# Optimization experiments

Hardware: AMD Instinct MI355X
Metric: run time of the kernel (lower is better)

Reference implementation:

```python
import jax, jax.numpy as jnp
import numpy as np

ANG = 7
N = ANG * ANG          # 49 views
CENTER = N // 2        # index 24 = central view
EDGE_C = 150.0
ALPHA = 0.1
CROP = 8
GAUSS = jnp.array([[0.0751, 0.1238, 0.0751],
                   [0.1238, 0.2042, 0.1238],
                   [0.0751, 0.1238, 0.0751]], dtype=jnp.float32)


def _edge_aware_smoothness(D, I):
    # D: [b,h,w] disparity; I: [b,3,h,w] center view
    gx = I[:, :, :, 1:] - I[:, :, :, :-1]
    gy = I[:, :, 1:, :] - I[:, :, :-1, :]
    wx = jnp.exp(-EDGE_C * jnp.mean(jnp.abs(gx), axis=1, keepdims=True))
    wy = jnp.exp(-EDGE_C * jnp.mean(jnp.abs(gy), axis=1, keepdims=True))
    Du = D[:, None]
    dgx = Du[:, :, :, 1:] - Du[:, :, :, :-1]
    dgy = Du[:, :, 1:, :] - Du[:, :, :-1, :]
    lx = jnp.mean((wx * jnp.abs(dgx))[:, :, CROP:-CROP, CROP:-CROP])
    ly = jnp.mean((wy * jnp.abs(dgy))[:, :, CROP:-CROP, CROP:-CROP])
    return (lx + ly) / 2.0


def _warp_all(pred, x):
    # Backward-warp each of the 49 views toward the center view using the
    # per-pixel disparity scaled by the view's angular offset (bilinear,
    # border-clamped) -- standard light-field warping (warp_all in the repo).
    # pred: [b,h,w]; x: [b,3,N,h,w] -> warped [b,3,N,h,w]
    b, c, n, h, w = x.shape
    off = jnp.arange(ANG, dtype=pred.dtype) - (ANG // 2)
    du = jnp.repeat(off, ANG)   # row (u) offset per view, [N]
    dv = jnp.tile(off, ANG)     # col (v) offset per view, [N]
    gy = jnp.arange(h, dtype=pred.dtype)[:, None]
    gx = jnp.arange(w, dtype=pred.dtype)[None, :]
    p = pred[:, None, :, :]                                # [b,1,h,w]
    cy = jnp.clip(gy[None, None] + p * du[None, :, None, None], 0.0, h - 1)
    cx = jnp.clip(gx[None, None] + p * dv[None, :, None, None], 0.0, w - 1)
    y0f = jnp.floor(cy); x0f = jnp.floor(cx)
    ty = (cy - y0f)[..., None]; tx = (cx - x0f)[..., None]
    y0 = y0f.astype(jnp.int32); x0 = x0f.astype(jnp.int32)
    y1 = jnp.minimum(y0 + 1, h - 1); x1 = jnp.minimum(x0 + 1, w - 1)
    img = jnp.transpose(x, (0, 2, 3, 4, 1)).reshape(b, n, h * w, c)

    def gather(yi, xi):
        idx = (yi * w + xi).reshape(b, n, h * w, 1)
        return jnp.take_along_axis(img, idx, axis=2).reshape(b, n, h, w, c)

    out = (gather(y0, x0) * (1 - ty) * (1 - tx)
           + gather(y0, x1) * (1 - ty) * tx
           + gather(y1, x0) * ty * (1 - tx)
           + gather(y1, x1) * ty * tx)
    return jnp.transpose(out, (0, 4, 1, 2, 3))


def _gauss_smooth_angular(cl):
    # cl [b,1,N,h,w]: 3x3 gaussian conv over the 7x7 angular grid, replicate pad
    b, _, _, h, w = cl.shape
    g = cl.reshape(b, 1, ANG, ANG, h, w)
    g = jnp.pad(g, ((0, 0), (0, 0), (1, 1), (1, 1), (0, 0), (0, 0)), mode='edge')
    out = sum(GAUSS[i, j] * g[:, :, i:i + ANG, j:j + ANG]
              for i in range(3) for j in range(3))
    return out.reshape(b, 1, N, h, w)


def _forward(pred, x, y, epoch):
    b, u, v, h, w, c = x.shape
    # 'b u v h w c -> b c (u v) h w'
    xr = jnp.transpose(x, (0, 5, 1, 2, 3, 4)).reshape(b, c, N, h, w)
    center = xr[:, :, CENTER]                               # [b,3,h,w]
    grad_loss = _edge_aware_smoothness(pred, center)
    warped = _warp_all(pred, xr)                            # [b,3,N,h,w]
    color_loss = jnp.mean(jnp.abs(warped - warped[:, :, CENTER:CENTER + 1]),
                          axis=1, keepdims=True)            # [b,1,N,h,w]
    if epoch > 0:
        gauss = jax.lax.stop_gradient(_gauss_smooth_angular(color_loss))
        idx = jnp.argsort(-gauss, axis=2)                   # descending
        sorted_cl = jnp.take_along_axis(color_loss, idx, axis=2)
    else:
        sorted_cl = -jnp.sort(-color_loss, axis=2)
    yb = y[:, None, None, :, :]
    ar = jnp.arange(N, dtype=y.dtype)[None, None, :, None, None]
    mask = (ar > yb).astype(color_loss.dtype) / (N - yb) * N
    if epoch > 0:
        mask = jax.lax.stop_gradient(mask)                  # torch no_grad branch
    cl = jnp.mean((sorted_cl * mask)[..., CROP:-CROP, CROP:-CROP])
    return cl + grad_loss * ALPHA


def setup_inputs():
    key = jax.random.key(0)
    k1, k2, k3 = jax.random.split(key, 3)
    b, h, w = 4, 256, 256
    pred = jax.random.normal(k1, (b, h, w), dtype=jnp.float32)
    x = jax.random.uniform(k2, (b, ANG, ANG, h, w, 3), dtype=jnp.float32)
    y = jax.random.uniform(k3, (b, h, w), dtype=jnp.float32) * 24.0  # keep ~half views
    return {"pred": pred, "x": x, "y": y, "epoch": 5}


def reference(pred, x, y, epoch):
    return _forward(pred, x, y, epoch)
```

## Files before the change

### kernel.cpp

```cpp
#include <hip/hip_runtime.h>
#include <math.h>

#define NV    49
#define Himg  256
#define Wimg  256
#define RW    240
#define RWH   (RW*RW)
#define NPIX  (4*RWH)
#define ROWF  (Wimg*3)
#define IMGF  (Himg*Wimg*3)
#define NBLK  (NPIX/64)


#define CL7(a) ((a)<0?0:((a)>6?6:(a)))

#define DO_VIEW(UC, VC) { \
    const float* s0p = xv + ((UC)*7 + (VC)) * IMGF + ro0 + co[VC]; \
    const float* s1p = xv + ((UC)*7 + (VC)) * IMGF + ro1 + co[VC]; \
    float s0[6], s1[6]; \
    __builtin_memcpy(s0, s0p, 24); \
    __builtin_memcpy(s1, s1p, 24); \
    float tx = txv[VC]; \
    float h0 = s0[0] + tx*(s0[3]-s0[0]); \
    float h1 = s0[1] + tx*(s0[4]-s0[1]); \
    float h2 = s0[2] + tx*(s0[5]-s0[2]); \
    float k0 = s1[0] + tx*(s1[3]-s1[0]); \
    float k1 = s1[1] + tx*(s1[4]-s1[1]); \
    float k2 = s1[2] + tx*(s1[5]-s1[2]); \
    float o0 = h0 + ty*(k0-h0); \
    float o1 = h1 + ty*(k1-h1); \
    float o2 = h2 + ty*(k2-h2); \
    mycl[(UC)*7+(VC)] = (fabsf(o0-c0)+fabsf(o1-c1)+fabsf(o2-c2)) * (1.0f/3.0f); \
}

#define DO_U(UC) { \
    float cy = fminf(fmaxf((float)yy + p * (float)((UC)-3), 0.0f), 255.0f); \
    float y0f = floorf(cy); \
    float ty = cy - y0f; \
    int iy0 = (int)y0f; \
    int iy1 = min(iy0+1, 255); \
    int ro0 = iy0*ROWF, ro1 = iy1*ROWF; \
    DO_VIEW(UC,0) DO_VIEW(UC,1) DO_VIEW(UC,2) DO_VIEW(UC,3) \
    DO_VIEW(UC,4) DO_VIEW(UC,5) DO_VIEW(UC,6) \
}

#define GV(UC,VC) myg[(UC)*7+(VC)] = \
    0.0751f*mycl[CL7((UC)-1)*7+CL7((VC)-1)] + 0.1238f*mycl[CL7((UC)-1)*7+(VC)] + 0.0751f*mycl[CL7((UC)-1)*7+CL7((VC)+1)] + \
    0.1238f*mycl[(UC)*7+CL7((VC)-1)]        + 0.2042f*mycl[(UC)*7+(VC)]        + 0.1238f*mycl[(UC)*7+CL7((VC)+1)] + \
    0.0751f*mycl[CL7((UC)+1)*7+CL7((VC)-1)] + 0.1238f*mycl[CL7((UC)+1)*7+(VC)] + 0.0751f*mycl[CL7((UC)+1)*7+CL7((VC)+1)];

#define GU(UC) GV(UC,0) GV(UC,1) GV(UC,2) GV(UC,3) GV(UC,4) GV(UC,5) GV(UC,6)

__global__ __launch_bounds__(256) void color_kernel(
    const float* __restrict__ pred, const float* __restrict__ x,
    const float* __restrict__ y, const int* __restrict__ epoch_p,
    double* __restrict__ acc)
{
    __shared__ float s_cl[64 * NV];
    __shared__ float s_g [64 * NV];
    __shared__ float sred[4];

    const int tid = threadIdx.x;
    const int pix = tid & 63;
    const int sub = tid >> 6;

    int lb  = (blockIdx.x & 7) * (NBLK/8) + (blockIdx.x >> 3);
    int pid = lb * 64 + pix;
    int b   = pid / RWH;
    int rem = pid - b * RWH;
    int ry  = rem / RW;
    int yy  = 8 + ry;
    int xx  = 8 + (rem - ry * RW);

    int pidx = (b * Himg + yy) * Wimg + xx;
    float p = pred[pidx];

    const float* xv    = x + (size_t)b * (49 * IMGF);
    const float* cbase = xv + (24 * IMGF) + (yy * Wimg + xx) * 3;
    float c0 = cbase[0], c1 = cbase[1], c2 = cbase[2];

    float* mycl = s_cl + pix * NV;
    float* myg  = s_g  + pix * NV;

    int co[7]; float txv[7];
    #pragma unroll
    for (int vv = 0; vv < 7; vv++) {
        float cx = fminf(fmaxf((float)xx + p * (float)(vv-3), 0.0f), 255.0f);
        float x0f = floorf(cx);
        float tx = cx - x0f;
        int ix0 = (int)x0f;
        if (ix0 >= 255) { ix0 = 254; tx = 1.0f; }
        co[vv] = ix0 * 3; txv[vv] = tx;
    }

    if (sub == 0)      { DO_U(0) DO_U(4) }
    else if (sub == 1) { DO_U(1) DO_U(5) }
    else if (sub == 2) { DO_U(2) DO_U(6) }
    else {
        DO_U(3)
        float lx = 0.0f, ly = 0.0f;
        if (xx <= 246) {
            float q6[6]; __builtin_memcpy(q6, cbase, 24);
            float wx = __expf(-50.0f * (fabsf(q6[3]-c0) + fabsf(q6[4]-c1) + fabsf(q6[5]-c2)));
            lx = wx * fabsf(pred[pidx + 1] - p);
        }
        if (yy <= 246) {
            float r0 = cbase[ROWF], r1 = cbase[ROWF+1], r2 = cbase[ROWF+2];
            float wy = __expf(-50.0f * (fabsf(r0-c0) + fabsf(r1-c1) + fabsf(r2-c2)));
            ly = wy * fabsf(pred[pidx + Wimg] - p);
        }
        #pragma unroll
        for (int off = 32; off > 0; off >>= 1) {
            lx += __shfl_down(lx, off);
            ly += __shfl_down(ly, off);
        }
        if ((tid & 63) == 0) {
            atomicAdd(acc + 1, (double)lx);
            atomicAdd(acc + 2, (double)ly);
        }
    }
    __syncthreads();

    const int epoch = *epoch_p;

    if (epoch > 0) {
        if (sub == 0)      { GU(0) GU(4) }
        else if (sub == 1) { GU(1) GU(5) }
        else if (sub == 2) { GU(2) GU(6) }
        else               { GU(3) }
    }
    __syncthreads();

    const float* key = (epoch > 0) ? myg : mycl;
    float yval = y[pidx];

    unsigned long long kn[13];
    int cnt[13];
    #pragma unroll
    for (int i = 0; i < 13; i++) {
        int n = sub + 4*i;
        if (n < NV) {
            unsigned int bb = __float_as_uint(key[n]);
            kn[i] = (((unsigned long long)bb) << 8) | (unsigned long long)(255 - n);
        } else kn[i] = ~0ULL;
        cnt[i] = 0;
    }
    for (int m = 0; m < NV; m++) {
        unsigned int bm = __float_as_uint(key[m]);
        unsigned long long km = (((unsigned long long)bm) << 8) | (unsigned long long)(255 - m);
        #pragma unroll
        for (int i = 0; i < 13; i++)
            cnt[i] += (km > kn[i]) ? 1 : 0;
    }
    float tail = 0.0f;
    #pragma unroll
    for (int i = 0; i < 13; i++) {
        int n = sub + 4*i;
        if (n < NV)
            tail += ((float)cnt[i] > yval) ? mycl[n] : 0.0f;
    }
    float contrib = tail * (49.0f / (49.0f - yval));

    #pragma unroll
    for (int off = 32; off > 0; off >>= 1)
        contrib += __shfl_down(contrib, off);
    if ((tid & 63) == 0) sred[sub] = contrib;
    __syncthreads();
    if (tid == 0)
        atomicAdd(acc + 0, (double)(sred[0] + sred[1] + sred[2] + sred[3]));
}

__global__ void finalize_kernel(const double* __restrict__ acc,
                                float* __restrict__ out)
{
    double cl = acc[0] / 11289600.0;
    double gl = (acc[1] + acc[2]) / (2.0 * 229440.0);
    out[0] = (float)(cl + 0.1 * gl);
}

extern "C" void kernel_launch(void* const* d_in, const int* in_sizes, int n_in,
                              void* d_out, int out_size, void* d_ws, size_t ws_size,
                              hipStream_t stream)
{
    const float* pred  = (const float*)d_in[0];
    const float* x     = (const float*)d_in[1];
    const float* y     = (const float*)d_in[2];
    const int*   epoch = (const int*)d_in[3];
    double* acc = (double*)d_ws;

    hipMemsetAsync(acc, 0, 3 * sizeof(double), stream);
    color_kernel<<<NBLK, 256, 0, stream>>>(pred, x, y, epoch, acc);
    finalize_kernel<<<1, 1, 0, stream>>>(acc, (float*)d_out);
}
```

Measured before the change: 325.7 us.

## Use seven wavefronts per block, one per angular row, balancing work

The block grows from 4 to 7 wavefronts, so each wavefront handles exactly one angular row of 7 views for warping, Gaussian smoothing and rank counting. Before, one wavefront did one row and the other three did two rows each, which left the work unbalanced. Each wavefront's color losses stay in registers for the tail sum, and the wavefront index is made uniform with readfirstlane so the per-row loops are not compiled as divergent branches. The larger block raises threads per block and may change register pressure and occupancy.

```diff
diff --git a/kernel.cpp b/kernel.cpp
--- a/kernel.cpp
+++ b/kernel.cpp
@@ -12,57 +12,18 @@
 #define NBLK  (NPIX/64)
 
 
-#define CL7(a) ((a)<0?0:((a)>6?6:(a)))
-
-#define DO_VIEW(UC, VC) { \
-    const float* s0p = xv + ((UC)*7 + (VC)) * IMGF + ro0 + co[VC]; \
-    const float* s1p = xv + ((UC)*7 + (VC)) * IMGF + ro1 + co[VC]; \
-    float s0[6], s1[6]; \
-    __builtin_memcpy(s0, s0p, 24); \
-    __builtin_memcpy(s1, s1p, 24); \
-    float tx = txv[VC]; \
-    float h0 = s0[0] + tx*(s0[3]-s0[0]); \
-    float h1 = s0[1] + tx*(s0[4]-s0[1]); \
-    float h2 = s0[2] + tx*(s0[5]-s0[2]); \
-    float k0 = s1[0] + tx*(s1[3]-s1[0]); \
-    float k1 = s1[1] + tx*(s1[4]-s1[1]); \
-    float k2 = s1[2] + tx*(s1[5]-s1[2]); \
-    float o0 = h0 + ty*(k0-h0); \
-    float o1 = h1 + ty*(k1-h1); \
-    float o2 = h2 + ty*(k2-h2); \
-    mycl[(UC)*7+(VC)] = (fabsf(o0-c0)+fabsf(o1-c1)+fabsf(o2-c2)) * (1.0f/3.0f); \
-}
-
-#define DO_U(UC) { \
-    float cy = fminf(fmaxf((float)yy + p * (float)((UC)-3), 0.0f), 255.0f); \
-    float y0f = floorf(cy); \
-    float ty = cy - y0f; \
-    int iy0 = (int)y0f; \
-    int iy1 = min(iy0+1, 255); \
-    int ro0 = iy0*ROWF, ro1 = iy1*ROWF; \
-    DO_VIEW(UC,0) DO_VIEW(UC,1) DO_VIEW(UC,2) DO_VIEW(UC,3) \
-    DO_VIEW(UC,4) DO_VIEW(UC,5) DO_VIEW(UC,6) \
-}
-
-#define GV(UC,VC) myg[(UC)*7+(VC)] = \
-    0.0751f*mycl[CL7((UC)-1)*7+CL7((VC)-1)] + 0.1238f*mycl[CL7((UC)-1)*7+(VC)] + 0.0751f*mycl[CL7((UC)-1)*7+CL7((VC)+1)] + \
-    0.1238f*mycl[(UC)*7+CL7((VC)-1)]        + 0.2042f*mycl[(UC)*7+(VC)]        + 0.1238f*mycl[(UC)*7+CL7((VC)+1)] + \
-    0.0751f*mycl[CL7((UC)+1)*7+CL7((VC)-1)] + 0.1238f*mycl[CL7((UC)+1)*7+(VC)] + 0.0751f*mycl[CL7((UC)+1)*7+CL7((VC)+1)];
-
-#define GU(UC) GV(UC,0) GV(UC,1) GV(UC,2) GV(UC,3) GV(UC,4) GV(UC,5) GV(UC,6)
-
-__global__ __launch_bounds__(256) void color_kernel(
+__global__ __launch_bounds__(448) void color_kernel(
     const float* __restrict__ pred, const float* __restrict__ x,
     const float* __restrict__ y, const int* __restrict__ epoch_p,
     double* __restrict__ acc)
 {
     __shared__ float s_cl[64 * NV];
     __shared__ float s_g [64 * NV];
-    __shared__ float sred[4];
+    __shared__ float sred[8];
 
     const int tid = threadIdx.x;
     const int pix = tid & 63;
-    const int sub = tid >> 6;
+    const int sub = __builtin_amdgcn_readfirstlane(tid >> 6);
 
     int lb  = (blockIdx.x & 7) * (NBLK/8) + (blockIdx.x >> 3);
     int pid = lb * 64 + pix;
@@ -74,6 +35,7 @@
 
     int pidx = (b * Himg + yy) * Wimg + xx;
     float p = pred[pidx];
+    const int epoch = *epoch_p;
 
     const float* xv    = x + (size_t)b * (49 * IMGF);
     const float* cbase = xv + (24 * IMGF) + (yy * Wimg + xx) * 3;
@@ -93,11 +55,39 @@
         co[vv] = ix0 * 3; txv[vv] = tx;
     }
 
-    if (sub == 0)      { DO_U(0) DO_U(4) }
-    else if (sub == 1) { DO_U(1) DO_U(5) }
-    else if (sub == 2) { DO_U(2) DO_U(6) }
-    else {
-        DO_U(3)
+    float creg[7];
+    {
+        float cy = fminf(fmaxf((float)yy + p * (float)(sub-3), 0.0f), 255.0f);
+        float y0f = floorf(cy);
+        float ty = cy - y0f;
+        int iy0 = (int)y0f;
+        int iy1 = min(iy0+1, 255);
+        int ro0 = iy0*ROWF, ro1 = iy1*ROWF;
+        const float* vbase = xv + sub * 7 * IMGF;
+        #pragma unroll
+        for (int vv = 0; vv < 7; vv++) {
+            const float* s0p = vbase + vv*IMGF + ro0 + co[vv];
+            const float* s1p = vbase + vv*IMGF + ro1 + co[vv];
+            float s0[6], s1[6];
+            __builtin_memcpy(s0, s0p, 24);
+            __builtin_memcpy(s1, s1p, 24);
+            float tx = txv[vv];
+            float h0 = s0[0] + tx*(s0[3]-s0[0]);
+            float h1 = s0[1] + tx*(s0[4]-s0[1]);
+            float h2 = s0[2] + tx*(s0[5]-s0[2]);
+            float k0 = s1[0] + tx*(s1[3]-s1[0]);
+            float k1 = s1[1] + tx*(s1[4]-s1[1]);
+            float k2 = s1[2] + tx*(s1[5]-s1[2]);
+            float o0 = h0 + ty*(k0-h0);
+            float o1 = h1 + ty*(k1-h1);
+            float o2 = h2 + ty*(k2-h2);
+            float cl = (fabsf(o0-c0)+fabsf(o1-c1)+fabsf(o2-c2)) * (1.0f/3.0f);
+            creg[vv] = cl;
+            mycl[sub*7 + vv] = cl;
+        }
+    }
+
+    if (sub == 3) {
         float lx = 0.0f, ly = 0.0f;
         if (xx <= 246) {
             float q6[6]; __builtin_memcpy(q6, cbase, 24);
@@ -114,60 +104,68 @@
             lx += __shfl_down(lx, off);
             ly += __shfl_down(ly, off);
         }
-        if ((tid & 63) == 0) {
+        if (pix == 0) {
             atomicAdd(acc + 1, (double)lx);
             atomicAdd(acc + 2, (double)ly);
         }
     }
     __syncthreads();
 
-    const int epoch = *epoch_p;
-
     if (epoch > 0) {
-        if (sub == 0)      { GU(0) GU(4) }
-        else if (sub == 1) { GU(1) GU(5) }
-        else if (sub == 2) { GU(2) GU(6) }
-        else               { GU(3) }
+        const int um1 = (sub > 0) ? sub-1 : 0;
+        const int up1 = (sub < 6) ? sub+1 : 6;
+        const float* rm = mycl + um1*7;
+        const float* rc = mycl + sub*7;
+        const float* rp = mycl + up1*7;
+        #pragma unroll
+        for (int vv = 0; vv < 7; vv++) {
+            const int vm = (vv > 0) ? vv-1 : 0;
+            const int vp = (vv < 6) ? vv+1 : 6;
+            myg[sub*7 + vv] =
+                0.0751f*rm[vm] + 0.1238f*rm[vv] + 0.0751f*rm[vp] +
+                0.1238f*rc[vm] + 0.2042f*rc[vv] + 0.1238f*rc[vp] +
+                0.0751f*rp[vm] + 0.1238f*rp[vv] + 0.0751f*rp[vp];
+        }
     }
     __syncthreads();
 
     const float* key = (epoch > 0) ? myg : mycl;
     float yval = y[pidx];
 
-    unsigned long long kn[13];
-    int cnt[13];
+    unsigned long long kn[7];
+    int cnt[7];
     #pragma unroll
-    for (int i = 0; i < 13; i++) {
-        int n = sub + 4*i;
-        if (n < NV) {
-            unsigned int bb = __float_as_uint(key[n]);
-            kn[i] = (((unsigned long long)bb) << 8) | (unsigned long long)(255 - n);
-        } else kn[i] = ~0ULL;
+    for (int i = 0; i < 7; i++) {
+        int n = sub*7 + i;
+        unsigned int bb = __float_as_uint(key[n]);
+        kn[i] = (((unsigned long long)bb) << 8) | (unsigned long long)(255 - n);
         cnt[i] = 0;
     }
+    #pragma unroll 7
     for (int m = 0; m < NV; m++) {
         unsigned int bm = __float_as_uint(key[m]);
         unsigned long long km = (((unsigned long long)bm) << 8) | (unsigned long long)(255 - m);
         #pragma unroll
-        for (int i = 0; i < 13; i++)
+        for (int i = 0; i < 7; i++)
             cnt[i] += (km > kn[i]) ? 1 : 0;
     }
     float tail = 0.0f;
     #pragma unroll
-    for (int i = 0; i < 13; i++) {
-        int n = sub + 4*i;
-        if (n < NV)
-            tail += ((float)cnt[i] > yval) ? mycl[n] : 0.0f;
-    }
+    for (int i = 0; i < 7; i++)
+        tail += ((float)cnt[i] > yval) ? creg[i] : 0.0f;
     float contrib = tail * (49.0f / (49.0f - yval));
 
     #pragma unroll
     for (int off = 32; off > 0; off >>= 1)
         contrib += __shfl_down(contrib, off);
-    if ((tid & 63) == 0) sred[sub] = contrib;
+    if (pix == 0) sred[sub] = contrib;
     __syncthreads();
-    if (tid == 0)
-        atomicAdd(acc + 0, (double)(sred[0] + sred[1] + sred[2] + sred[3]));
+    if (tid == 0) {
+        double s = 0.0;
+        #pragma unroll
+        for (int i = 0; i < 7; i++) s += (double)sred[i];
+        atomicAdd(acc + 0, s);
+    }
 }
 
 __global__ void finalize_kernel(const double* __restrict__ acc,
@@ -189,6 +187,6 @@
     double* acc = (double*)d_ws;
 
     hipMemsetAsync(acc, 0, 3 * sizeof(double), stream);
-    color_kernel<<<NBLK, 256, 0, stream>>>(pred, x, y, epoch, acc);
+    color_kernel<<<NBLK, 448, 0, stream>>>(pred, x, y, epoch, acc);
     finalize_kernel<<<1, 1, 0, stream>>>(acc, (float*)d_out);
 }
```

Measured after the change: 329.0 us. Within noise of the previous version (+1.0%).
